# Kernel optimization log

Measured on AMD Instinct MI355X. Metric: run time of the kernel, lower is better.

The kernel has to match this reference:

```python
import jax, jax.numpy as jnp
import numpy as np

B, S, D, FF, H = 4, 512, 768, 3072, 12
HD = D // H
PH, KD, NK, KNN, MEM = 4, 512, 128, 32, 128 * 128
HALF = KD // 2
EPS = 1e-12


def _ln(x, g, b):
    m = jnp.mean(x, axis=-1, keepdims=True)
    v = jnp.var(x, axis=-1, keepdims=True)
    return (x - m) * jax.lax.rsqrt(v + EPS) * g + b


def setup_inputs() -> dict:
    key = jax.random.key(0)
    ks = iter(jax.random.split(key, 32))
    sc = 0.02
    rn = lambda shape, s=sc: jax.random.normal(next(ks), shape, dtype=jnp.float32) * s
    inp = {
        "x": jax.random.normal(next(ks), (B, S, D), dtype=jnp.float32),
        "Wq_attn": rn((D, D)), "bq_attn": jnp.zeros((D,), jnp.float32),
        "Wk_attn": rn((D, D)), "bk_attn": jnp.zeros((D,), jnp.float32),
        "Wv_attn": rn((D, D)), "bv_attn": jnp.zeros((D,), jnp.float32),
        "Wo_attn": rn((D, D)), "bo_attn": jnp.zeros((D,), jnp.float32),
        "ln1_g": jnp.ones((D,), jnp.float32), "ln1_b": jnp.zeros((D,), jnp.float32),
        "Wi": rn((D, FF)), "bi": jnp.zeros((FF,), jnp.float32),
        "Wd": rn((FF, D)), "bd": jnp.zeros((D,), jnp.float32),
        "ln2_g": jnp.ones((D,), jnp.float32), "ln2_b": jnp.zeros((D,), jnp.float32),
        "Wpq": rn((FF, PH * KD)), "bpq": jnp.zeros((PH * KD,), jnp.float32),
        "pkm_keys": rn((PH, 2, NK, HALF), 1.0 / np.sqrt(HALF)),
        "pkm_values": rn((MEM, D), 1.0 / np.sqrt(D)),
    }
    return inp


def _pkm(t, Wpq, bpq, keys, values):
    # t: [T, FF] -> [T, D] via product-key memory lookup
    T = t.shape[0]
    q = (t @ Wpq + bpq).reshape(T, PH, KD)
    q1, q2 = q[..., :HALF], q[..., HALF:]                        # [T, PH, HALF]
    s1 = jnp.einsum("thd,hnd->thn", q1, keys[:, 0])              # [T, PH, NK]
    s2 = jnp.einsum("thd,hnd->thn", q2, keys[:, 1])
    v1, i1 = jax.lax.top_k(s1, KNN)                              # [T, PH, KNN]
    v2, i2 = jax.lax.top_k(s2, KNN)
    cart = (v1[..., :, None] + v2[..., None, :]).reshape(T, PH, KNN * KNN)
    sc, idx = jax.lax.top_k(cart, KNN)                           # [T, PH, KNN]
    sel1 = jnp.take_along_axis(i1, idx // KNN, axis=-1)
    sel2 = jnp.take_along_axis(i2, idx % KNN, axis=-1)
    ind = sel1 * NK + sel2                                       # [T, PH, KNN] in [0, MEM)
    w = jax.nn.softmax(sc, axis=-1)
    return jnp.einsum("thk,thkd->td", w, values[ind])            # sum over heads and knn


def reference(x, Wq_attn, bq_attn, Wk_attn, bk_attn, Wv_attn, bv_attn,
              Wo_attn, bo_attn, ln1_g, ln1_b, Wi, bi, Wd, bd,
              ln2_g, ln2_b, Wpq, bpq, pkm_keys, pkm_values):
    # --- self-attention ---
    def heads(y):
        return y.reshape(B, S, H, HD).transpose(0, 2, 1, 3)      # [B, H, S, HD]
    q = heads(x @ Wq_attn + bq_attn)
    k = heads(x @ Wk_attn + bk_attn)
    v = heads(x @ Wv_attn + bv_attn)
    scores = jnp.einsum("bhsd,bhtd->bhst", q, k) / np.sqrt(HD)
    a = jax.nn.softmax(scores, axis=-1)
    ctx = jnp.einsum("bhst,bhtd->bhsd", a, v).transpose(0, 2, 1, 3).reshape(B, S, D)
    attn_out = _ln(ctx @ Wo_attn + bo_attn + x, ln1_g, ln1_b)
    # --- intermediate ---
    inter = jax.nn.gelu(attn_out @ Wi + bi, approximate=False)   # [B, S, FF]
    # --- ResM output: dense + PKM + residual -> LN ---
    dense = inter @ Wd + bd                                      # [B, S, D]
    pkm = _pkm(inter.reshape(B * S, FF), Wpq, bpq, pkm_keys, pkm_values).reshape(B, S, D)
    return _ln(dense + pkm + attn_out, ln2_g, ln2_b)
```

## Files before the change

### kernel.cpp

```cpp
#include <hip/hip_runtime.h>
#include <math.h>

constexpr int CB = 4, CS = 512, CD = 768, CFF = 3072, CH = 12, CHD = 64;
constexpr int CT = CB * CS;
constexpr int PH = 4, KD = 512, NK = 128, KNN = 32, HALF = 256;

typedef __attribute__((ext_vector_type(8))) short short8_t;
typedef __attribute__((ext_vector_type(4))) float f32x4;

__device__ __forceinline__ unsigned short f2bf(float f) {
    unsigned int u = __float_as_uint(f);
    return (unsigned short)((u + 0x7FFF + ((u >> 16) & 1)) >> 16);
}
__device__ __forceinline__ float bf2f(unsigned short h) {
    return __uint_as_float(((unsigned)h) << 16);
}

__device__ __forceinline__ void ld_lds16(const unsigned short* g, unsigned short* l) {
    __builtin_amdgcn_global_load_lds(
        (const __attribute__((address_space(1))) void*)g,
        (__attribute__((address_space(3))) void*)l, 16, 0, 0);
}

__global__ __launch_bounds__(256) void cvt_bf16x4(const float* __restrict__ in,
    unsigned short* __restrict__ out, int n4)
{
    for (int i = blockIdx.x * 256 + threadIdx.x; i < n4; i += gridDim.x * 256) {
        float4 v = ((const float4*)in)[i];
        ushort4 o = { f2bf(v.x), f2bf(v.y), f2bf(v.z), f2bf(v.w) };
        ((ushort4*)out)[i] = o;
    }
}

__global__ __launch_bounds__(256) void prep_kernel(
    const float* __restrict__ Wq, const float* __restrict__ Wk,
    const float* __restrict__ Wv, const float* __restrict__ Wo,
    const float* __restrict__ Wi, const float* __restrict__ Wd,
    const float* __restrict__ Wpq, unsigned short* __restrict__ wt,
    const float* __restrict__ x, unsigned short* __restrict__ xb,
    const float* __restrict__ keys, unsigned short* __restrict__ keysb)
{
    const int b = blockIdx.x, tid = threadIdx.x;
    if (b < 6528) {
        __shared__ unsigned short ts[32][72];
        const float* W; unsigned short* WT; int K, N, tile;
        if (b < 1152) {
            int z = b / 288; tile = b - z * 288;
            W = (z == 0) ? Wq : (z == 1) ? Wk : (z == 2) ? Wv : Wo;
            WT = wt + (size_t)z * 589824; K = 768; N = 768;
        } else if (b < 2304) {
            tile = b - 1152; W = Wi; WT = wt + 4 * 589824; K = 768; N = 3072;
        } else if (b < 3456) {
            tile = b - 2304; W = Wd; WT = wt + 4 * 589824 + 2359296; K = 3072; N = 768;
        } else {
            tile = b - 3456; W = Wpq; WT = wt + 4 * 589824 + 2 * 2359296; K = 3072; N = 2048;
        }
        const int nx = N >> 5;
        const int n0 = (tile % nx) * 32, k0 = (tile / nx) * 64;
        const int c = tid & 31, rr = tid >> 5;
#pragma unroll
        for (int i = 0; i < 8; i++) {
            int r = rr + i * 8;
            ts[c][r] = f2bf(W[(size_t)(k0 + r) * N + n0 + c]);
        }
        __syncthreads();
        const int nn = tid >> 3, kc = tid & 7;
        uint4 v = *(const uint4*)&ts[nn][kc * 8];
        *(uint4*)&WT[(size_t)(n0 + nn) * K + k0 + kc * 8] = v;
    } else if (b < 8064) {
        const int i = (b - 6528) * 256 + tid;
        float4 v = ((const float4*)x)[i];
        ushort4 o = { f2bf(v.x), f2bf(v.y), f2bf(v.z), f2bf(v.w) };
        ((ushort4*)xb)[i] = o;
    } else {
        const int i = (b - 8064) * 256 + tid;
        float4 v = ((const float4*)keys)[i];
        ushort4 o = { f2bf(v.x), f2bf(v.y), f2bf(v.z), f2bf(v.w) };
        ((ushort4*)keysb)[i] = o;
    }
}

template<int TM, int CMODE, int ACT, int PKMM, int BMODE>
__global__ __launch_bounds__(256) void gemm_lds(
    const unsigned short* __restrict__ A, const unsigned short* __restrict__ BT,
    const float* __restrict__ b0, const float* __restrict__ b1,
    const float* __restrict__ b2,
    void* __restrict__ Cg, void* __restrict__ Cg2,
    int M, int N, int K, int lda, int ldc, int ldc2)
{
    __shared__ unsigned short As[2][TM * 64];
    __shared__ unsigned short Bs[2][128 * 64];
    const int tid = threadIdx.x, lane = tid & 63, w = tid >> 6;
    const int l15 = lane & 15, l4 = lane >> 4;
    const int wr = w >> 1, wc = w & 1;
    constexpr int NI = (TM + 31) / 32 > 1 ? TM / 32 : 1;

    int bx = blockIdx.x, by = blockIdx.y;
    {
        const int nx = gridDim.x, nwg = nx * gridDim.y;
        if ((nwg & 7) == 0) {
            int flat = by * nx + bx;
            const int cpx = nwg >> 3;
            flat = (flat & 7) * cpx + (flat >> 3);
            bx = flat % nx; by = flat / nx;
        }
    }

    size_t aoff = 0, boff = 0, coff = 0;
    if (PKMM) {
        int z = blockIdx.z;
        aoff = (size_t)(z >> 1) * KD + (size_t)(z & 1) * HALF;
        boff = (size_t)z * NK * HALF;
        coff = (size_t)z * NK;
    }
    const int rowA0 = by * TM, rowB0 = bx * 128;

    const int sr = lane >> 3, sc = lane & 7;
    const int scg = sc ^ sr;
    const int cx = l15 & 7;

    f32x4 acc[NI][4];
#pragma unroll
    for (int i = 0; i < NI; i++)
#pragma unroll
        for (int j = 0; j < 4; j++) acc[i][j] = (f32x4){0.f, 0.f, 0.f, 0.f};

    auto STAGE = [&](int t, int buf) {
        const int k0 = t * 64;
        if (TM == 128) {
#pragma unroll
            for (int i = 0; i < 4; i++) {
                const int r0 = w * 32 + i * 8;
                ld_lds16(&A[aoff + (size_t)(rowA0 + r0 + sr) * lda + k0 + scg * 8],
                         &As[buf][r0 * 64]);
            }
        } else if (TM == 64) {
#pragma unroll
            for (int i = 0; i < 2; i++) {
                const int r0 = w * 16 + i * 8;
                ld_lds16(&A[aoff + (size_t)(rowA0 + r0 + sr) * lda + k0 + scg * 8],
                         &As[buf][r0 * 64]);
            }
        } else {
            const int r0 = w * 8;
            ld_lds16(&A[aoff + (size_t)(rowA0 + r0 + sr) * lda + k0 + scg * 8],
                     &As[buf][r0 * 64]);
        }
#pragma unroll
        for (int i = 0; i < 4; i++) {
            const int r0 = w * 32 + i * 8;
            ld_lds16(&BT[boff + (size_t)(rowB0 + r0 + sr) * K + k0 + scg * 8],
                     &Bs[buf][r0 * 64]);
        }
    };

    const int NT = K / 64;
    STAGE(0, 0);
    for (int t = 0; t < NT; ++t) {
        const int cur = t & 1;
        if (t + 1 < NT) {
            STAGE(t + 1, cur ^ 1);
            if constexpr (TM == 128)     asm volatile("s_waitcnt vmcnt(8)" ::: "memory");
            else if constexpr (TM == 64) asm volatile("s_waitcnt vmcnt(6)" ::: "memory");
            else                         asm volatile("s_waitcnt vmcnt(5)" ::: "memory");
        } else {
            asm volatile("s_waitcnt vmcnt(0)" ::: "memory");
        }
        __builtin_amdgcn_sched_barrier(0);
        __builtin_amdgcn_s_barrier();
        __builtin_amdgcn_sched_barrier(0);

        short8_t af[2][NI], bf[2][4];
#pragma unroll
        for (int h = 0; h < 2; h++) {
            const int co = ((l4 + 4 * h) ^ cx) * 8;
#pragma unroll
            for (int i = 0; i < NI; i++)
                af[h][i] = *(const short8_t*)&As[cur][(wr * (TM / 2) + i * 16 + l15) * 64 + co];
#pragma unroll
            for (int j = 0; j < 4; j++)
                bf[h][j] = *(const short8_t*)&Bs[cur][(wc * 64 + j * 16 + l15) * 64 + co];
        }
#pragma unroll
        for (int h = 0; h < 2; h++)
#pragma unroll
            for (int i = 0; i < NI; i++)
#pragma unroll
                for (int j = 0; j < 4; j++)
                    acc[i][j] = __builtin_amdgcn_mfma_f32_16x16x32_bf16(af[h][i], bf[h][j], acc[i][j], 0, 0, 0);
        __builtin_amdgcn_sched_barrier(0);
        __builtin_amdgcn_s_barrier();
        __builtin_amdgcn_sched_barrier(0);
    }

#pragma unroll
    for (int i = 0; i < NI; i++) {
#pragma unroll
        for (int j = 0; j < 4; j++) {
            const int row = rowA0 + wr * (TM / 2) + i * 16 + l4 * 4;
            const int col = rowB0 + wc * 64 + j * 16 + l15;
            float bv;
            if (PKMM) bv = 0.f;
            else if (BMODE == 0) bv = b0[col];
            else if (BMODE == 1) bv = (col < 768) ? b0[col] : (col < 1536 ? b1[col - 768] : b2[col - 1536]);
            else bv = (col < 768) ? b0[col] : b1[col - 768];
#pragma unroll
            for (int jj = 0; jj < 4; jj++) {
                float v = acc[i][j][jj] + bv;
                if (ACT == 1) v = 0.5f * v * (1.0f + erff(v * 0.70710678118654752f));
                if (CMODE == 0)
                    ((float*)Cg)[coff + (size_t)(row + jj) * ldc + col] = v;
                else if (CMODE == 1)
                    ((unsigned short*)Cg)[coff + (size_t)(row + jj) * ldc + col] = f2bf(v);
                else {
                    if (col < 768)
                        ((float*)Cg)[(size_t)(row + jj) * ldc + col] = v;
                    else
                        ((unsigned short*)Cg2)[(size_t)(row + jj) * ldc2 + (col - 768)] = f2bf(v);
                }
            }
        }
    }
}

constexpr int AST = 72;

__global__ __launch_bounds__(256) void attn_mfma(const unsigned short* __restrict__ qkv,
    unsigned short* __restrict__ ctx)
{
    __shared__ unsigned short Qs[64 * AST], Ks[64 * AST], Vt[64 * AST], Ss[64 * AST];
    const int tid = threadIdx.x, lane = tid & 63, w = tid >> 6;
    const int l15 = lane & 15, l4 = lane >> 4;
    const int h = blockIdx.y, b = blockIdx.z, q0 = blockIdx.x * 64;
    const int tb0 = b * CS;

#pragma unroll
    for (int it = 0; it < 2; ++it) {
        int e = it * 256 + tid, r = e >> 3, c = e & 7;
        *(uint4*)&Qs[r * AST + c * 8] =
            *(const uint4*)&qkv[(size_t)(tb0 + q0 + r) * 2304 + h * 64 + c * 8];
    }
    f32x4 accO[4];
    float mreg[4], lreg[4];
#pragma unroll
    for (int j = 0; j < 4; j++) accO[j] = (f32x4){0.f, 0.f, 0.f, 0.f};
#pragma unroll
    for (int r = 0; r < 4; r++) { mreg[r] = -1e30f; lreg[r] = 0.f; }
    __syncthreads();
    const short8_t aq0 = *(const short8_t*)&Qs[(w * 16 + l15) * AST + l4 * 8];
    const short8_t aq1 = *(const short8_t*)&Qs[(w * 16 + l15) * AST + 32 + l4 * 8];

    for (int kt = 0; kt < 8; ++kt) {
        __syncthreads();
#pragma unroll
        for (int it = 0; it < 2; ++it) {
            int e = it * 256 + tid, r = e >> 3, c = e & 7;
            *(uint4*)&Ks[r * AST + c * 8] =
                *(const uint4*)&qkv[(size_t)(tb0 + kt * 64 + r) * 2304 + 768 + h * 64 + c * 8];
            uint4 vv = *(const uint4*)&qkv[(size_t)(tb0 + kt * 64 + r) * 2304 + 1536 + h * 64 + c * 8];
            const unsigned short* pv = (const unsigned short*)&vv;
            const int rc = (((r >> 3) + c) & 7) * 8 + (r & 7);
#pragma unroll
            for (int e2 = 0; e2 < 8; ++e2)
                Vt[(c * 8 + e2) * AST + rc] = pv[e2];
        }
        __syncthreads();

        f32x4 sc[4];
#pragma unroll
        for (int j = 0; j < 4; j++) sc[j] = (f32x4){0.f, 0.f, 0.f, 0.f};
#pragma unroll
        for (int j = 0; j < 4; j++) {
            short8_t bk0 = *(const short8_t*)&Ks[(j * 16 + l15) * AST + l4 * 8];
            short8_t bk1 = *(const short8_t*)&Ks[(j * 16 + l15) * AST + 32 + l4 * 8];
            sc[j] = __builtin_amdgcn_mfma_f32_16x16x32_bf16(aq0, bk0, sc[j], 0, 0, 0);
            sc[j] = __builtin_amdgcn_mfma_f32_16x16x32_bf16(aq1, bk1, sc[j], 0, 0, 0);
        }

        float cf[4];
#pragma unroll
        for (int r = 0; r < 4; r++) {
            float s0 = sc[0][r] * 0.125f, s1 = sc[1][r] * 0.125f;
            float s2 = sc[2][r] * 0.125f, s3 = sc[3][r] * 0.125f;
            float mt = fmaxf(fmaxf(s0, s1), fmaxf(s2, s3));
            mt = fmaxf(mt, __shfl_xor(mt, 1));
            mt = fmaxf(mt, __shfl_xor(mt, 2));
            mt = fmaxf(mt, __shfl_xor(mt, 4));
            mt = fmaxf(mt, __shfl_xor(mt, 8));
            float mo = mreg[r], mn = fmaxf(mo, mt);
            float c = __expf(mo - mn);
            mreg[r] = mn; cf[r] = c;
            float p0 = __expf(s0 - mn), p1 = __expf(s1 - mn);
            float p2 = __expf(s2 - mn), p3 = __expf(s3 - mn);
            float ps = p0 + p1 + p2 + p3;
            ps += __shfl_xor(ps, 1);
            ps += __shfl_xor(ps, 2);
            ps += __shfl_xor(ps, 4);
            ps += __shfl_xor(ps, 8);
            lreg[r] = lreg[r] * c + ps;
            const int qrow = (w * 16 + l4 * 4 + r) * AST;
            Ss[qrow + l15]      = f2bf(p0);
            Ss[qrow + 16 + l15] = f2bf(p1);
            Ss[qrow + 32 + l15] = f2bf(p2);
            Ss[qrow + 48 + l15] = f2bf(p3);
        }
#pragma unroll
        for (int j = 0; j < 4; j++) {
            accO[j][0] *= cf[0]; accO[j][1] *= cf[1];
            accO[j][2] *= cf[2]; accO[j][3] *= cf[3];
        }

        const short8_t ap0 = *(const short8_t*)&Ss[(w * 16 + l15) * AST + l4 * 8];
        const short8_t ap1 = *(const short8_t*)&Ss[(w * 16 + l15) * AST + 32 + l4 * 8];
#pragma unroll
        for (int j = 0; j < 4; j++) {
            const int d = j * 16 + l15, dc = d >> 3;
            short8_t bv0 = *(const short8_t*)&Vt[d * AST + (((l4    ) + dc) & 7) * 8];
            short8_t bv1 = *(const short8_t*)&Vt[d * AST + (((l4 + 4) + dc) & 7) * 8];
            accO[j] = __builtin_amdgcn_mfma_f32_16x16x32_bf16(ap0, bv0, accO[j], 0, 0, 0);
            accO[j] = __builtin_amdgcn_mfma_f32_16x16x32_bf16(ap1, bv1, accO[j], 0, 0, 0);
        }
    }

    float inv[4];
#pragma unroll
    for (int r = 0; r < 4; r++) inv[r] = 1.0f / lreg[r];
#pragma unroll
    for (int j = 0; j < 4; j++)
#pragma unroll
        for (int r = 0; r < 4; r++)
            ctx[(size_t)(tb0 + q0 + w * 16 + l4 * 4 + r) * CD + h * 64 + j * 16 + l15] =
                f2bf(accO[j][r] * inv[r]);
}

__global__ __launch_bounds__(256) void ln_kernel(float* __restrict__ out,
    unsigned short* __restrict__ outb,
    const float* __restrict__ a, int lda,
    const float* __restrict__ b2,
    const float* __restrict__ g, const float* __restrict__ bb)
{
    const int t = blockIdx.x, tid = threadIdx.x;
    __shared__ float buf[CD];
    __shared__ float red[256];
    float l = 0.f;
    for (int d = tid; d < CD; d += 256) {
        float v = a[(size_t)t * lda + d];
        if (b2) v += b2[(size_t)t * CD + d];
        buf[d] = v; l += v;
    }
    red[tid] = l; __syncthreads();
    for (int o = 128; o > 0; o >>= 1) { if (tid < o) red[tid] += red[tid + o]; __syncthreads(); }
    const float mean = red[0] * (1.0f / CD); __syncthreads();
    float l2 = 0.f;
    for (int d = tid; d < CD; d += 256) { float dd = buf[d] - mean; l2 += dd * dd; }
    red[tid] = l2; __syncthreads();
    for (int o = 128; o > 0; o >>= 1) { if (tid < o) red[tid] += red[tid + o]; __syncthreads(); }
    const float inv = rsqrtf(red[0] * (1.0f / CD) + 1e-12f);
    for (int d = tid; d < CD; d += 256) {
        float v = (buf[d] - mean) * inv * g[d] + bb[d];
        out[(size_t)t * CD + d] = v;
        if (outb) outb[(size_t)t * CD + d] = f2bf(v);
    }
}

__device__ const unsigned char CCNT[32] = {32,16,10,8,6,5,4,4,3,3,2,2,2,2,2,2,
                                           1,1,1,1,1,1,1,1,1,1,1,1,1,1,1,1};

__global__ __launch_bounds__(128) void pkm_topk_kernel(const float* __restrict__ sc,
    float* __restrict__ w, int* __restrict__ ind)
{
    const int gid = blockIdx.x;
    const int tid = threadIdx.x;
    __shared__ float sv[256];
    __shared__ int   si_[256];
    __shared__ float cv[128];
    __shared__ int   ci[128];

    const float* s = sc + (size_t)gid * 256;
    sv[tid] = s[tid];             si_[tid] = tid;
    sv[tid + 128] = s[tid + 128]; si_[tid + 128] = tid;
    __syncthreads();

    for (int k = 2; k <= 128; k <<= 1) {
        for (int j = k >> 1; j > 0; j >>= 1) {
            const int hh = tid >> 6, p = tid & 63;
            const int i = ((p & ~(j - 1)) << 1) | (p & (j - 1));
            const int l = i | j;
            const int bi_ = hh * 128 + i, bl = hh * 128 + l;
            float av = sv[bi_], bv2 = sv[bl];
            int   ai = si_[bi_], bx = si_[bl];
            const bool agtb = (av > bv2) || (av == bv2 && ai < bx);
            const bool desc = ((i & k) == 0);
            if (agtb != desc) { sv[bi_] = bv2; sv[bl] = av; si_[bi_] = bx; si_[bl] = ai; }
            __syncthreads();
        }
    }

    {
        float val; int fi;
        if (tid < 119) {
            int tt = tid, ii = 0;
            while (tt >= (int)CCNT[ii]) { tt -= CCNT[ii]; ii++; }
            val = sv[ii] + sv[128 + tt];
            fi = ii * 32 + tt;
        } else { val = -3.0e38f; fi = 0x7FFFFFF; }
        cv[tid] = val; ci[tid] = fi;
    }
    __syncthreads();

    for (int k = 2; k <= 128; k <<= 1) {
        for (int j = k >> 1; j > 0; j >>= 1) {
            if (tid < 64) {
                const int p = tid;
                const int i = ((p & ~(j - 1)) << 1) | (p & (j - 1));
                const int l = i | j;
                float av = cv[i], bv2 = cv[l];
                int   ai = ci[i], bx = ci[l];
                const bool agtb = (av > bv2) || (av == bv2 && ai < bx);
                const bool desc = ((i & k) == 0);
                if (agtb != desc) { cv[i] = bv2; cv[l] = av; ci[i] = bx; ci[l] = ai; }
            }
            __syncthreads();
        }
    }

    if (tid < 32) {
        const float mx = cv[0];
        float e = __expf(cv[tid] - mx);
        float s2 = e;
        for (int o = 16; o > 0; o >>= 1) s2 += __shfl_xor(s2, o);
        const int fi = ci[tid];
        const int ii = fi >> 5, jj = fi & 31;
        w[(size_t)gid * KNN + tid] = e / s2;
        ind[(size_t)gid * KNN + tid] = si_[ii] * NK + si_[128 + jj];
    }
}

__global__ __launch_bounds__(256) void ln2_pkm_kernel(
    const float* __restrict__ dense, const float* __restrict__ attnf,
    const float* __restrict__ wgt, const int* __restrict__ ind,
    const unsigned short* __restrict__ valb,
    const float* __restrict__ g, const float* __restrict__ bb,
    float* __restrict__ out)
{
    const int t = blockIdx.x, tid = threadIdx.x;
    __shared__ float ws[PH * KNN];
    __shared__ int   is[PH * KNN];
    __shared__ float red[256];
    if (tid < PH * KNN) {
        ws[tid] = wgt[(size_t)t * PH * KNN + tid];
        is[tid] = ind[(size_t)t * PH * KNN + tid];
    }
    __syncthreads();
    float a0 = 0.f, a1 = 0.f, a2 = 0.f;
#pragma unroll 4
    for (int i = 0; i < PH * KNN; i++) {
        const unsigned short* vr = valb + (size_t)is[i] * CD;
        const float wv = ws[i];
        a0 = fmaf(wv, bf2f(vr[tid]), a0);
        a1 = fmaf(wv, bf2f(vr[tid + 256]), a1);
        a2 = fmaf(wv, bf2f(vr[tid + 512]), a2);
    }
    const size_t base = (size_t)t * CD;
    float v0 = a0 + dense[base + tid]       + attnf[base + tid];
    float v1 = a1 + dense[base + tid + 256] + attnf[base + tid + 256];
    float v2 = a2 + dense[base + tid + 512] + attnf[base + tid + 512];

    red[tid] = v0 + v1 + v2; __syncthreads();
    for (int o = 128; o > 0; o >>= 1) { if (tid < o) red[tid] += red[tid + o]; __syncthreads(); }
    const float mean = red[0] * (1.0f / CD); __syncthreads();
    float d0 = v0 - mean, d1 = v1 - mean, d2 = v2 - mean;
    red[tid] = d0 * d0 + d1 * d1 + d2 * d2; __syncthreads();
    for (int o = 128; o > 0; o >>= 1) { if (tid < o) red[tid] += red[tid + o]; __syncthreads(); }
    const float inv = rsqrtf(red[0] * (1.0f / CD) + 1e-12f);
    out[base + tid]       = d0 * inv * g[tid]       + bb[tid];
    out[base + tid + 256] = d1 * inv * g[tid + 256] + bb[tid + 256];
    out[base + tid + 512] = d2 * inv * g[tid + 512] + bb[tid + 512];
}

extern "C" void kernel_launch(void* const* d_in, const int* in_sizes, int n_in,
                              void* d_out, int out_size, void* d_ws, size_t ws_size,
                              hipStream_t stream)
{
    const float* x      = (const float*)d_in[0];
    const float* Wq     = (const float*)d_in[1];
    const float* bq     = (const float*)d_in[2];
    const float* Wk     = (const float*)d_in[3];
    const float* bk     = (const float*)d_in[4];
    const float* Wv     = (const float*)d_in[5];
    const float* bv     = (const float*)d_in[6];
    const float* Wo     = (const float*)d_in[7];
    const float* bo     = (const float*)d_in[8];
    const float* ln1_g  = (const float*)d_in[9];
    const float* ln1_b  = (const float*)d_in[10];
    const float* Wi     = (const float*)d_in[11];
    const float* bi     = (const float*)d_in[12];
    const float* Wd     = (const float*)d_in[13];
    const float* bd     = (const float*)d_in[14];
    const float* ln2_g  = (const float*)d_in[15];
    const float* ln2_b  = (const float*)d_in[16];
    const float* Wpq    = (const float*)d_in[17];
    const float* bpq    = (const float*)d_in[18];
    const float* keys   = (const float*)d_in[19];
    const float* values = (const float*)d_in[20];

    char* W = (char*)d_ws;
    unsigned short* qkvb  = (unsigned short*)(W + 0);
    float*          sbuf  = (float*)(W + 0);
    float*          attnf = (float*)(W + 9437184);
    unsigned short* ctxb  = (unsigned short*)(W + 15728640);
    unsigned short* interb= (unsigned short*)(W + 15728640);
    float*          wgt   = (float*)(W + 15728640);
    int*            ind   = (int*)(W + 16777216);
    unsigned short* xb    = (unsigned short*)(W + 28311552);
    float*          woout = (float*)(W + 28311552);
    float*          dense = (float*)(W + 28311552);
    unsigned short* attnb = (unsigned short*)(W + 34603008);
    unsigned short* pqb   = (unsigned short*)(W + 37748736);
    unsigned short* keysb = (unsigned short*)(W + 46137344);
    unsigned short* wt    = (unsigned short*)(W + 46661632);
    unsigned short* valb  = (unsigned short*)(W + 46661632);

    const dim3 blk(256);
    const size_t WOFF = 589824;

    prep_kernel<<<8320, blk, 0, stream>>>(Wq, Wk, Wv, Wo, Wi, Wd, Wpq, wt,
                                          x, xb, keys, keysb);

    gemm_lds<64, 1, 0, 0, 1><<<dim3(18, 32), blk, 0, stream>>>(
        xb, wt, bq, bk, bv, qkvb, nullptr, CT, 2304, CD, CD, 2304, 0);

    attn_mfma<<<dim3(8, 12, 4), blk, 0, stream>>>(qkvb, ctxb);

    gemm_lds<32, 0, 0, 0, 0><<<dim3(6, 64), blk, 0, stream>>>(
        ctxb, wt + 3 * WOFF, bo, nullptr, nullptr, woout, nullptr, CT, CD, CD, CD, CD, 0);
    ln_kernel<<<CT, blk, 0, stream>>>(attnf, attnb, woout, CD, x, ln1_g, ln1_b);

    gemm_lds<64, 1, 1, 0, 0><<<dim3(24, 32), blk, 0, stream>>>(
        attnb, wt + 4 * WOFF, bi, nullptr, nullptr, interb, nullptr, CT, CFF, CD, CD, CFF, 0);

    gemm_lds<64, 2, 0, 0, 2><<<dim3(22, 32), blk, 0, stream>>>(
        interb, wt + 4 * WOFF + 2359296, bd, bpq, nullptr, dense, pqb, CT, 2816, CFF, CFF, CD, 2048);

    cvt_bf16x4<<<2048, blk, 0, stream>>>(values, valb, (NK * NK * CD) / 4);

    gemm_lds<32, 0, 0, 1, 0><<<dim3(1, 64, 8), blk, 0, stream>>>(
        pqb, keysb, nullptr, nullptr, nullptr, sbuf, nullptr, CT, NK, HALF, 2048, PH * 2 * NK, 0);

    pkm_topk_kernel<<<CT * PH, dim3(128), 0, stream>>>(sbuf, wgt, ind);

    ln2_pkm_kernel<<<CT, blk, 0, stream>>>(dense, attnf, wgt, ind, valb,
                                           ln2_g, ln2_b, (float*)d_out);
}
```

Before: 247.4 us.

## Store PKM value table in FP8 and prefetch K/V tiles in attention

The PKM value table is now converted to FP8 instead of bf16, and a new fused gather plus LayerNorm kernel decodes packed FP8 values with four values per thread and a shuffle-based reduction. The aim is to halve the bytes moved by the convert pass and by the random-row gather. Separately, the attention kernel prefetches the next K/V tile into registers while the current tile is being computed, so global load latency overlaps with the MFMA work. FP8 cuts value precision sharply and may break the accuracy tolerance.

```diff
diff --git a/kernel.cpp b/kernel.cpp
--- a/kernel.cpp
+++ b/kernel.cpp
@@ -1,5 +1,11 @@
 #include <hip/hip_runtime.h>
 #include <math.h>
+
+#if __has_builtin(__builtin_amdgcn_cvt_pk_f32_fp8) && __has_builtin(__builtin_amdgcn_cvt_pk_fp8_f32)
+#define HAS_FP8 1
+#else
+#define HAS_FP8 0
+#endif
 
 constexpr int CB = 4, CS = 512, CD = 768, CFF = 3072, CH = 12, CHD = 64;
 constexpr int CT = CB * CS;
@@ -7,6 +13,7 @@
 
 typedef __attribute__((ext_vector_type(8))) short short8_t;
 typedef __attribute__((ext_vector_type(4))) float f32x4;
+typedef __attribute__((ext_vector_type(2))) float f32x2;
 
 __device__ __forceinline__ unsigned short f2bf(float f) {
     unsigned int u = __float_as_uint(f);
@@ -31,6 +38,20 @@
         ((ushort4*)out)[i] = o;
     }
 }
+
+#if HAS_FP8
+__global__ __launch_bounds__(256) void cvt_fp8x4(const float* __restrict__ in,
+    unsigned* __restrict__ out, int n4)
+{
+    for (int i = blockIdx.x * 256 + threadIdx.x; i < n4; i += gridDim.x * 256) {
+        float4 v = ((const float4*)in)[i];
+        int p = 0;
+        p = __builtin_amdgcn_cvt_pk_fp8_f32(v.x, v.y, p, false);
+        p = __builtin_amdgcn_cvt_pk_fp8_f32(v.z, v.w, p, true);
+        out[i] = (unsigned)p;
+    }
+}
+#endif
 
 __global__ __launch_bounds__(256) void prep_kernel(
     const float* __restrict__ Wq, const float* __restrict__ Wk,
@@ -233,6 +254,7 @@
     const int l15 = lane & 15, l4 = lane >> 4;
     const int h = blockIdx.y, b = blockIdx.z, q0 = blockIdx.x * 64;
     const int tb0 = b * CS;
+    const int rS = tid >> 3, cS = tid & 7;
 
 #pragma unroll
     for (int it = 0; it < 2; ++it) {
@@ -246,24 +268,33 @@
     for (int j = 0; j < 4; j++) accO[j] = (f32x4){0.f, 0.f, 0.f, 0.f};
 #pragma unroll
     for (int r = 0; r < 4; r++) { mreg[r] = -1e30f; lreg[r] = 0.f; }
+
+    uint4 kr[2], vr[2];
+    auto LOADKV = [&](int kt) {
+#pragma unroll
+        for (int it = 0; it < 2; ++it) {
+            int e = it * 256 + tid, r = e >> 3, c = e & 7;
+            kr[it] = *(const uint4*)&qkv[(size_t)(tb0 + kt * 64 + r) * 2304 + 768 + h * 64 + c * 8];
+            vr[it] = *(const uint4*)&qkv[(size_t)(tb0 + kt * 64 + r) * 2304 + 1536 + h * 64 + c * 8];
+        }
+    };
+    LOADKV(0);
     __syncthreads();
     const short8_t aq0 = *(const short8_t*)&Qs[(w * 16 + l15) * AST + l4 * 8];
     const short8_t aq1 = *(const short8_t*)&Qs[(w * 16 + l15) * AST + 32 + l4 * 8];
 
     for (int kt = 0; kt < 8; ++kt) {
-        __syncthreads();
 #pragma unroll
         for (int it = 0; it < 2; ++it) {
             int e = it * 256 + tid, r = e >> 3, c = e & 7;
-            *(uint4*)&Ks[r * AST + c * 8] =
-                *(const uint4*)&qkv[(size_t)(tb0 + kt * 64 + r) * 2304 + 768 + h * 64 + c * 8];
-            uint4 vv = *(const uint4*)&qkv[(size_t)(tb0 + kt * 64 + r) * 2304 + 1536 + h * 64 + c * 8];
-            const unsigned short* pv = (const unsigned short*)&vv;
+            *(uint4*)&Ks[r * AST + c * 8] = kr[it];
+            const unsigned short* pv = (const unsigned short*)&vr[it];
             const int rc = (((r >> 3) + c) & 7) * 8 + (r & 7);
 #pragma unroll
             for (int e2 = 0; e2 < 8; ++e2)
                 Vt[(c * 8 + e2) * AST + rc] = pv[e2];
         }
+        if (kt + 1 < 8) LOADKV(kt + 1);
         __syncthreads();
 
         f32x4 sc[4];
@@ -320,6 +351,7 @@
             accO[j] = __builtin_amdgcn_mfma_f32_16x16x32_bf16(ap0, bv0, accO[j], 0, 0, 0);
             accO[j] = __builtin_amdgcn_mfma_f32_16x16x32_bf16(ap1, bv1, accO[j], 0, 0, 0);
         }
+        __syncthreads();
     }
 
     float inv[4];
@@ -477,6 +509,72 @@
     out[base + tid + 256] = d1 * inv * g[tid + 256] + bb[tid + 256];
     out[base + tid + 512] = d2 * inv * g[tid + 512] + bb[tid + 512];
 }
+
+#if HAS_FP8
+__global__ __launch_bounds__(192) void ln2_pkm_f8(
+    const float* __restrict__ dense, const float* __restrict__ attnf,
+    const float* __restrict__ wgt, const int* __restrict__ ind,
+    const unsigned char* __restrict__ valf8,
+    const float* __restrict__ g, const float* __restrict__ bb,
+    float* __restrict__ out)
+{
+    const int t = blockIdx.x, tid = threadIdx.x;
+    __shared__ float ws[PH * KNN];
+    __shared__ int   is[PH * KNN];
+    __shared__ float red[2];
+    if (tid < PH * KNN) {
+        ws[tid] = wgt[(size_t)t * PH * KNN + tid];
+        is[tid] = ind[(size_t)t * PH * KNN + tid];
+    }
+    __syncthreads();
+    float a0 = 0.f, a1 = 0.f, a2 = 0.f, a3 = 0.f;
+#pragma unroll 4
+    for (int i = 0; i < PH * KNN; i++) {
+        unsigned pv = *(const unsigned*)(valf8 + (size_t)is[i] * CD + tid * 4);
+        const float wv = ws[i];
+        f32x2 lo = __builtin_amdgcn_cvt_pk_f32_fp8(pv, false);
+        f32x2 hi = __builtin_amdgcn_cvt_pk_f32_fp8(pv, true);
+        a0 = fmaf(wv, lo.x, a0);
+        a1 = fmaf(wv, lo.y, a1);
+        a2 = fmaf(wv, hi.x, a2);
+        a3 = fmaf(wv, hi.y, a3);
+    }
+    const size_t base = (size_t)t * CD + tid * 4;
+    float4 dv = *(const float4*)(dense + base);
+    float4 av = *(const float4*)(attnf + base);
+    float v0 = a0 + dv.x + av.x, v1 = a1 + dv.y + av.y;
+    float v2 = a2 + dv.z + av.z, v3 = a3 + dv.w + av.w;
+
+    __shared__ float rbuf[192];
+    rbuf[tid] = v0 + v1 + v2 + v3; __syncthreads();
+    if (tid < 64) {
+        float s = rbuf[tid] + rbuf[tid + 64] + rbuf[tid + 128];
+        s += __shfl_xor(s, 32); s += __shfl_xor(s, 16); s += __shfl_xor(s, 8);
+        s += __shfl_xor(s, 4);  s += __shfl_xor(s, 2);  s += __shfl_xor(s, 1);
+        if (tid == 0) red[0] = s;
+    }
+    __syncthreads();
+    const float mean = red[0] * (1.0f / CD);
+    float d0 = v0 - mean, d1 = v1 - mean, d2 = v2 - mean, d3 = v3 - mean;
+    rbuf[tid] = d0 * d0 + d1 * d1 + d2 * d2 + d3 * d3; __syncthreads();
+    if (tid < 64) {
+        float s = rbuf[tid] + rbuf[tid + 64] + rbuf[tid + 128];
+        s += __shfl_xor(s, 32); s += __shfl_xor(s, 16); s += __shfl_xor(s, 8);
+        s += __shfl_xor(s, 4);  s += __shfl_xor(s, 2);  s += __shfl_xor(s, 1);
+        if (tid == 0) red[1] = s;
+    }
+    __syncthreads();
+    const float inv = rsqrtf(red[1] * (1.0f / CD) + 1e-12f);
+    float4 gv = *(const float4*)(g + tid * 4);
+    float4 bv = *(const float4*)(bb + tid * 4);
+    float4 o;
+    o.x = d0 * inv * gv.x + bv.x;
+    o.y = d1 * inv * gv.y + bv.y;
+    o.z = d2 * inv * gv.z + bv.z;
+    o.w = d3 * inv * gv.w + bv.w;
+    *(float4*)(out + base) = o;
+}
+#endif
 
 extern "C" void kernel_launch(void* const* d_in, const int* in_sizes, int n_in,
                               void* d_out, int out_size, void* d_ws, size_t ws_size,
@@ -519,7 +617,7 @@
     unsigned short* pqb   = (unsigned short*)(W + 37748736);
     unsigned short* keysb = (unsigned short*)(W + 46137344);
     unsigned short* wt    = (unsigned short*)(W + 46661632);
-    unsigned short* valb  = (unsigned short*)(W + 46661632);
+    void*           valq  = (void*)(W + 46661632);
 
     const dim3 blk(256);
     const size_t WOFF = 589824;
@@ -542,13 +640,22 @@
     gemm_lds<64, 2, 0, 0, 2><<<dim3(22, 32), blk, 0, stream>>>(
         interb, wt + 4 * WOFF + 2359296, bd, bpq, nullptr, dense, pqb, CT, 2816, CFF, CFF, CD, 2048);
 
-    cvt_bf16x4<<<2048, blk, 0, stream>>>(values, valb, (NK * NK * CD) / 4);
+#if HAS_FP8
+    cvt_fp8x4<<<2048, blk, 0, stream>>>(values, (unsigned*)valq, (NK * NK * CD) / 4);
+#else
+    cvt_bf16x4<<<2048, blk, 0, stream>>>(values, (unsigned short*)valq, (NK * NK * CD) / 4);
+#endif
 
     gemm_lds<32, 0, 0, 1, 0><<<dim3(1, 64, 8), blk, 0, stream>>>(
         pqb, keysb, nullptr, nullptr, nullptr, sbuf, nullptr, CT, NK, HALF, 2048, PH * 2 * NK, 0);
 
     pkm_topk_kernel<<<CT * PH, dim3(128), 0, stream>>>(sbuf, wgt, ind);
 
-    ln2_pkm_kernel<<<CT, blk, 0, stream>>>(dense, attnf, wgt, ind, valb,
-                                           ln2_g, ln2_b, (float*)d_out);
-}
+#if HAS_FP8
+    ln2_pkm_f8<<<CT, dim3(192), 0, stream>>>(dense, attnf, wgt, ind,
+        (const unsigned char*)valq, ln2_g, ln2_b, (float*)d_out);
+#else
+    ln2_pkm_kernel<<<CT, blk, 0, stream>>>(dense, attnf, wgt, ind,
+        (const unsigned short*)valq, ln2_g, ln2_b, (float*)d_out);
+#endif
+}
```

New measurement: 249.1 us. Within noise of the previous version (+0.7%).
